# Performance work log

Measured on AMD Instinct MI355X. Metric: run time of the kernel, lower is better.

The kernel has to match this reference:

```python
import jax, jax.numpy as jnp
import numpy as np

EPS = 1e-5

def layer_norm(x, gamma, beta):
    mu = jnp.mean(x, axis=-1, keepdims=True)
    var = jnp.var(x, axis=-1, keepdims=True)
    return (x - mu) * jax.lax.rsqrt(var + EPS) * gamma + beta

def setup_inputs() -> dict:
    key = jax.random.key(0)
    ks = jax.random.split(key, 4)
    B, L, D = 32, 4096, 768
    x = jax.random.normal(ks[0], (B, L, D), dtype=jnp.float32)
    w_kv = jax.random.normal(ks[1], (2 * D, D), dtype=jnp.float32) * (D ** -0.5)
    query = jax.random.normal(ks[2], (D,), dtype=jnp.float32)
    gamma1 = jnp.ones((D,), jnp.float32)
    beta1 = jnp.zeros((D,), jnp.float32)
    gamma2 = jnp.ones((D,), jnp.float32)
    beta2 = jnp.zeros((D,), jnp.float32)
    return {"x": x, "w_kv": w_kv, "query": query,
            "gamma1": gamma1, "beta1": beta1,
            "gamma2": gamma2, "beta2": beta2}

def reference(x, w_kv, query, gamma1, beta1, gamma2, beta2):
    B, L, D = x.shape
    H = 8
    Dh = D // H
    scale = Dh ** -0.5
    xn = layer_norm(x, gamma1, beta1)                      # [B,L,D]
    kv = jnp.einsum('bld,ed->ble', xn, w_kv)               # [B,L,2D]
    k, v = jnp.split(kv, 2, axis=-1)                       # [B,L,D] each
    k = k.reshape(B, L, H, Dh)                             # [B,L,H,Dh]
    v = v.reshape(B, L, H, Dh)
    q = query.reshape(H, Dh)                               # [H,Dh]
    dots = jnp.einsum('hd,blhd->bhl', q, k) * scale        # [B,H,L]
    attn = jax.nn.softmax(dots, axis=-1)                   # [B,H,L]
    out = jnp.einsum('bhl,blhd->bhd', attn, v)             # [B,H,Dh]
    out = out.reshape(B, D)                                # [B,D]
    return layer_norm(out, gamma2, beta2)
```

## Files before the change

### kernel.cpp

```cpp
#include <hip/hip_runtime.h>
#include <stdint.h>

#define DD 768
#define HN 8
#define LL 4096
#define BB 32
#define ROWS 64
#define NBLK (BB * LL / ROWS)
#define DEPTH 6
#define PSTR 772

#define GLOBAL_AS __attribute__((address_space(1)))
#define LDS_AS    __attribute__((address_space(3)))

#define DPP_STEP(x, ctrl, rmask, bc)                                           \
  x += __int_as_float(__builtin_amdgcn_update_dpp(                             \
      0, __float_as_int(x), (ctrl), (rmask), 0xf, (bc)))

__device__ __forceinline__ void wave_sum4(float& a, float& b, float& c, float& d) {
  DPP_STEP(a, 0x111, 0xf, true);  DPP_STEP(b, 0x111, 0xf, true);
  DPP_STEP(c, 0x111, 0xf, true);  DPP_STEP(d, 0x111, 0xf, true);
  DPP_STEP(a, 0x112, 0xf, true);  DPP_STEP(b, 0x112, 0xf, true);
  DPP_STEP(c, 0x112, 0xf, true);  DPP_STEP(d, 0x112, 0xf, true);
  DPP_STEP(a, 0x114, 0xf, true);  DPP_STEP(b, 0x114, 0xf, true);
  DPP_STEP(c, 0x114, 0xf, true);  DPP_STEP(d, 0x114, 0xf, true);
  DPP_STEP(a, 0x118, 0xf, true);  DPP_STEP(b, 0x118, 0xf, true);
  DPP_STEP(c, 0x118, 0xf, true);  DPP_STEP(d, 0x118, 0xf, true);
  DPP_STEP(a, 0x142, 0xa, false); DPP_STEP(b, 0x142, 0xa, false);
  DPP_STEP(c, 0x142, 0xa, false); DPP_STEP(d, 0x142, 0xa, false);
  DPP_STEP(a, 0x143, 0xc, false); DPP_STEP(b, 0x143, 0xc, false);
  DPP_STEP(c, 0x143, 0xc, false); DPP_STEP(d, 0x143, 0xc, false);
  a = __int_as_float(__builtin_amdgcn_readlane(__float_as_int(a), 63));
  b = __int_as_float(__builtin_amdgcn_readlane(__float_as_int(b), 63));
  c = __int_as_float(__builtin_amdgcn_readlane(__float_as_int(c), 63));
  d = __int_as_float(__builtin_amdgcn_readlane(__float_as_int(d), 63));
}

__device__ __forceinline__ void wave_sum2(float& a, float& b) {
  DPP_STEP(a, 0x111, 0xf, true);  DPP_STEP(b, 0x111, 0xf, true);
  DPP_STEP(a, 0x112, 0xf, true);  DPP_STEP(b, 0x112, 0xf, true);
  DPP_STEP(a, 0x114, 0xf, true);  DPP_STEP(b, 0x114, 0xf, true);
  DPP_STEP(a, 0x118, 0xf, true);  DPP_STEP(b, 0x118, 0xf, true);
  DPP_STEP(a, 0x142, 0xa, false); DPP_STEP(b, 0x142, 0xa, false);
  DPP_STEP(a, 0x143, 0xc, false); DPP_STEP(b, 0x143, 0xc, false);
  a = __int_as_float(__builtin_amdgcn_readlane(__float_as_int(a), 63));
  b = __int_as_float(__builtin_amdgcn_readlane(__float_as_int(b), 63));
}

__global__ __launch_bounds__(256) void k_qk(const float* __restrict__ wkv,
                                            const float* __restrict__ query,
                                            const float* __restrict__ gamma1,
                                            float* __restrict__ qkraw) {
  int h = blockIdx.x / 3;
  int d = (blockIdx.x % 3) * 256 + threadIdx.x;
  const float* wbase = wkv + (size_t)h * 96 * DD + d;
  const float* qb = query + h * 96;
  float acc = 0.f;
  #pragma unroll 8
  for (int i = 0; i < 96; ++i) acc = fmaf(qb[i], wbase[(size_t)i * DD], acc);
  qkraw[h * DD + d] = acc * 0.10206207261596577f * gamma1[d];
}

__global__ __launch_bounds__(64, 2) void k_main(
    const float* __restrict__ x, const float* __restrict__ qkraw,
    float* __restrict__ part) {
  const int lane = threadIdx.x;
  __shared__ float lds[DEPTH][DD];
  float* ring = &lds[0][0];

  float4 q[HN][3];
  #pragma unroll
  for (int h = 0; h < HN; ++h)
    #pragma unroll
    for (int j = 0; j < 3; ++j)
      q[h][j] = *reinterpret_cast<const float4*>(qkraw + h * DD + j * 256 + lane * 4);
  asm volatile("s_waitcnt vmcnt(0)" ::: "memory");

  {
    float m[HN];
    #pragma unroll
    for (int h = 0; h < HN; ++h) {
      float s = 0.f;
      #pragma unroll
      for (int j = 0; j < 3; ++j)
        s += q[h][j].x + q[h][j].y + q[h][j].z + q[h][j].w;
      m[h] = s;
    }
    wave_sum4(m[0], m[1], m[2], m[3]);
    wave_sum4(m[4], m[5], m[6], m[7]);
    #pragma unroll
    for (int h = 0; h < HN; ++h) {
      float mv = m[h] * (1.f / 768.f);
      #pragma unroll
      for (int j = 0; j < 3; ++j) {
        q[h][j].x -= mv; q[h][j].y -= mv; q[h][j].z -= mv; q[h][j].w -= mv;
      }
    }
  }

  float4 S[HN][3];
  float se[HN], ch[HN];
  #pragma unroll
  for (int h = 0; h < HN; ++h) {
    se[h] = 0.f; ch[h] = 0.f;
    #pragma unroll
    for (int j = 0; j < 3; ++j) S[h][j] = make_float4(0.f, 0.f, 0.f, 0.f);
  }

  const float* gbase = x + (size_t)blockIdx.x * ROWS * DD;

  #define STAGE(R, SLOT)                                                       \
    {                                                                          \
      const float* gt = gbase + (size_t)(R) * DD;                              \
      float* db = ring + (SLOT) * DD;                                          \
      _Pragma("unroll")                                                        \
      for (int i = 0; i < 3; ++i)                                              \
        __builtin_amdgcn_global_load_lds(                                      \
            (const GLOBAL_AS uint32_t*)(gt + i * 256 + lane * 4),              \
            (LDS_AS uint32_t*)(db + i * 256), 16, 0, 0);                       \
    }

  #define COMPUTE(SLOT)                                                        \
    {                                                                          \
      const float* row = ring + (SLOT) * DD;                                   \
      float4 c0 = *reinterpret_cast<const float4*>(row + lane * 4);            \
      float4 c1 = *reinterpret_cast<const float4*>(row + 256 + lane * 4);      \
      float4 c2 = *reinterpret_cast<const float4*>(row + 512 + lane * 4);      \
      float s1 = 0.f, s2 = 0.f;                                                \
      float dt[HN];                                                            \
      _Pragma("unroll") for (int h = 0; h < HN; ++h) dt[h] = 0.f;              \
      ACC4(c0, 0) ACC4(c1, 1) ACC4(c2, 2)                                      \
      wave_sum4(s1, s2, dt[0], dt[1]);                                         \
      wave_sum4(dt[2], dt[3], dt[4], dt[5]);                                   \
      wave_sum2(dt[6], dt[7]);                                                 \
      float mu   = s1 * (1.f / 768.f);                                         \
      float var  = fmaf(-mu, mu, s2 * (1.f / 768.f));                          \
      float rstd = rsqrtf(var + 1e-5f);                                        \
      float sh   = -mu * rstd;                                                 \
      float pe   = rstd * 1.44269504f;                                         \
      _Pragma("unroll")                                                        \
      for (int h = 0; h < HN; ++h) {                                           \
        float p = exp2f(dt[h] * pe);                                           \
        se[h] += p;                                                            \
        ch[h] = fmaf(p, sh, ch[h]);                                            \
        float a = p * rstd;                                                    \
        S[h][0].x = fmaf(a, c0.x, S[h][0].x);                                  \
        S[h][0].y = fmaf(a, c0.y, S[h][0].y);                                  \
        S[h][0].z = fmaf(a, c0.z, S[h][0].z);                                  \
        S[h][0].w = fmaf(a, c0.w, S[h][0].w);                                  \
        S[h][1].x = fmaf(a, c1.x, S[h][1].x);                                  \
        S[h][1].y = fmaf(a, c1.y, S[h][1].y);                                  \
        S[h][1].z = fmaf(a, c1.z, S[h][1].z);                                  \
        S[h][1].w = fmaf(a, c1.w, S[h][1].w);                                  \
        S[h][2].x = fmaf(a, c2.x, S[h][2].x);                                  \
        S[h][2].y = fmaf(a, c2.y, S[h][2].y);                                  \
        S[h][2].z = fmaf(a, c2.z, S[h][2].z);                                  \
        S[h][2].w = fmaf(a, c2.w, S[h][2].w);                                  \
      }                                                                        \
    }

#define ACC4(cv, J)                                                            \
      s1 += cv.x + cv.y + cv.z + cv.w;                                         \
      s2 = fmaf(cv.x, cv.x, s2); s2 = fmaf(cv.y, cv.y, s2);                    \
      s2 = fmaf(cv.z, cv.z, s2); s2 = fmaf(cv.w, cv.w, s2);                    \
      _Pragma("unroll")                                                        \
      for (int h = 0; h < HN; ++h) {                                           \
        dt[h] = fmaf(cv.x, q[h][J].x, dt[h]);                                  \
        dt[h] = fmaf(cv.y, q[h][J].y, dt[h]);                                  \
        dt[h] = fmaf(cv.z, q[h][J].z, dt[h]);                                  \
        dt[h] = fmaf(cv.w, q[h][J].w, dt[h]);                                  \
      }

  STAGE(0, 0) STAGE(1, 1) STAGE(2, 2) STAGE(3, 3) STAGE(4, 4)

  int sIn = 5, sCur = 0;
  #pragma unroll 1
  for (int r = 0; r <= ROWS - 6; ++r) {
    STAGE(r + 5, sIn)
    sIn = (sIn == DEPTH - 1) ? 0 : sIn + 1;
    asm volatile("s_waitcnt vmcnt(15)" ::: "memory");
    COMPUTE(sCur)
    sCur = (sCur == DEPTH - 1) ? 0 : sCur + 1;
  }
  asm volatile("s_waitcnt vmcnt(12)" ::: "memory");
  COMPUTE(sCur) sCur = (sCur == DEPTH - 1) ? 0 : sCur + 1;
  asm volatile("s_waitcnt vmcnt(9)" ::: "memory");
  COMPUTE(sCur) sCur = (sCur == DEPTH - 1) ? 0 : sCur + 1;
  asm volatile("s_waitcnt vmcnt(6)" ::: "memory");
  COMPUTE(sCur) sCur = (sCur == DEPTH - 1) ? 0 : sCur + 1;
  asm volatile("s_waitcnt vmcnt(3)" ::: "memory");
  COMPUTE(sCur) sCur = (sCur == DEPTH - 1) ? 0 : sCur + 1;
  asm volatile("s_waitcnt vmcnt(0)" ::: "memory");
  COMPUTE(sCur)

  #undef ACC4
  #undef COMPUTE
  #undef STAGE

  float* pb = part + (size_t)blockIdx.x * (HN * PSTR);
  #pragma unroll
  for (int h = 0; h < HN; ++h) {
    #pragma unroll
    for (int j = 0; j < 3; ++j) {
      float4 v = S[h][j];
      v.x += ch[h]; v.y += ch[h]; v.z += ch[h]; v.w += ch[h];
      *reinterpret_cast<float4*>(pb + h * PSTR + j * 256 + lane * 4) = v;
    }
  }
  if (lane == 0) {
    #pragma unroll
    for (int h = 0; h < HN; ++h) pb[h * PSTR + 768] = se[h];
  }
}

__global__ __launch_bounds__(256) void k_red(const float* __restrict__ part,
                                             const float* __restrict__ gamma1,
                                             const float* __restrict__ beta1,
                                             float* __restrict__ xbar) {
  int b = blockIdx.x >> 3;
  int h = blockIdx.x & 7;
  int t = threadIdx.x;
  const int CPB = LL / ROWS;
  const float* pb = part + ((size_t)b * CPB * HN + h) * PSTR;
  float se = 0.f, a0 = 0.f, a1 = 0.f, a2 = 0.f;
  #pragma unroll 4
  for (int i = 0; i < CPB; ++i) {
    const float* P = pb + (size_t)i * HN * PSTR;
    se += P[768];
    a0 += P[t];
    a1 += P[t + 256];
    a2 += P[t + 512];
  }
  float inv = 1.f / se;
  size_t ob = ((size_t)b * HN + h) * DD;
  xbar[ob + t]       = fmaf(gamma1[t],       a0 * inv, beta1[t]);
  xbar[ob + t + 256] = fmaf(gamma1[t + 256], a1 * inv, beta1[t + 256]);
  xbar[ob + t + 512] = fmaf(gamma1[t + 512], a2 * inv, beta1[t + 512]);
}

__global__ __launch_bounds__(256) void k_proj(
    const float* __restrict__ xbar, const float* __restrict__ wkv,
    float* __restrict__ outp) {
  int b  = blockIdx.x / 3;
  int gc = blockIdx.x % 3;
  int t  = threadIdx.x;
  __shared__ float xb[HN * DD];
  #pragma unroll
  for (int k = 0; k < 24; ++k) xb[k * 256 + t] = xbar[(size_t)b * HN * DD + k * 256 + t];
  __syncthreads();

  int g = gc * 256 + t;
  int h = g / 96;
  const float4* wrow = reinterpret_cast<const float4*>(wkv + (size_t)(DD + g) * DD);
  const float* xh = xb + h * DD;
  float acc = 0.f;
  #pragma unroll 4
  for (int e = 0; e < 192; ++e) {
    float4 w = wrow[e];
    acc = fmaf(w.x, xh[e * 4 + 0], acc);
    acc = fmaf(w.y, xh[e * 4 + 1], acc);
    acc = fmaf(w.z, xh[e * 4 + 2], acc);
    acc = fmaf(w.w, xh[e * 4 + 3], acc);
  }
  outp[(size_t)b * DD + g] = acc;
}

__global__ __launch_bounds__(768) void k_ln2(
    const float* __restrict__ outp, const float* __restrict__ gamma2,
    const float* __restrict__ beta2, float* __restrict__ out) {
  int b = blockIdx.x;
  int t = threadIdx.x;
  __shared__ float rs1[12], rs2[12];
  __shared__ float smu, srstd;
  float o = outp[(size_t)b * DD + t];
  float v1 = o, v2 = o * o;
  #pragma unroll
  for (int off = 1; off < 64; off <<= 1) {
    v1 += __shfl_xor(v1, off, 64);
    v2 += __shfl_xor(v2, off, 64);
  }
  int wv = t >> 6, ln = t & 63;
  if (ln == 0) { rs1[wv] = v1; rs2[wv] = v2; }
  __syncthreads();
  if (t == 0) {
    float s1 = 0.f, s2 = 0.f;
    #pragma unroll
    for (int w = 0; w < 12; ++w) { s1 += rs1[w]; s2 += rs2[w]; }
    float mu = s1 * (1.f / 768.f);
    float var = fmaf(-mu, mu, s2 * (1.f / 768.f));
    smu = mu;
    srstd = rsqrtf(var + 1e-5f);
  }
  __syncthreads();
  out[(size_t)b * DD + t] = fmaf((o - smu) * srstd, gamma2[t], beta2[t]);
}

extern "C" void kernel_launch(void* const* d_in, const int* in_sizes, int n_in,
                              void* d_out, int out_size, void* d_ws, size_t ws_size,
                              hipStream_t stream) {
  const float* x     = (const float*)d_in[0];
  const float* wkv   = (const float*)d_in[1];
  const float* query = (const float*)d_in[2];
  const float* g1    = (const float*)d_in[3];
  const float* b1    = (const float*)d_in[4];
  const float* g2    = (const float*)d_in[5];
  const float* b2    = (const float*)d_in[6];
  float* out = (float*)d_out;
  float* ws  = (float*)d_ws;

  float* qkraw = ws;
  float* part  = ws + 8192;
  float* xbar  = part + (size_t)NBLK * HN * PSTR;
  float* outp  = xbar + (size_t)BB * HN * DD;

  k_qk  <<<24,      256, 0, stream>>>(wkv, query, g1, qkraw);
  k_main<<<NBLK,    64,  0, stream>>>(x, qkraw, part);
  k_red <<<BB * HN, 256, 0, stream>>>(part, g1, b1, xbar);
  k_proj<<<BB * 3,  256, 0, stream>>>(xbar, wkv, outp);
  k_ln2 <<<BB,      768, 0, stream>>>(outp, g2, b2, out);
}
```

Measured before the change: 188.6 us.

## Process two rows per iteration with pair-granular triple-buffered LDS staging

The main loop now handles a pair of rows per iteration. Their dot-product and moment accumulations are interleaved, and all wave reductions are batched into five full four-value DPP reductions. Staging moves from a six-slot ring of single rows to three slots of row pairs. Each slot is refilled right after it is consumed, with waitcnt thresholds adjusted to match. The aim is more instruction-level parallelism and less reduction overhead per row, at the cost of higher register pressure and a shallower effective prefetch distance.

```diff
diff --git a/kernel.cpp b/kernel.cpp
--- a/kernel.cpp
+++ b/kernel.cpp
@@ -7,7 +7,7 @@
 #define BB 32
 #define ROWS 64
 #define NBLK (BB * LL / ROWS)
-#define DEPTH 6
+#define NP (ROWS / 2)
 #define PSTR 772
 
 #define GLOBAL_AS __attribute__((address_space(1)))
@@ -36,17 +36,6 @@
   d = __int_as_float(__builtin_amdgcn_readlane(__float_as_int(d), 63));
 }
 
-__device__ __forceinline__ void wave_sum2(float& a, float& b) {
-  DPP_STEP(a, 0x111, 0xf, true);  DPP_STEP(b, 0x111, 0xf, true);
-  DPP_STEP(a, 0x112, 0xf, true);  DPP_STEP(b, 0x112, 0xf, true);
-  DPP_STEP(a, 0x114, 0xf, true);  DPP_STEP(b, 0x114, 0xf, true);
-  DPP_STEP(a, 0x118, 0xf, true);  DPP_STEP(b, 0x118, 0xf, true);
-  DPP_STEP(a, 0x142, 0xa, false); DPP_STEP(b, 0x142, 0xa, false);
-  DPP_STEP(a, 0x143, 0xc, false); DPP_STEP(b, 0x143, 0xc, false);
-  a = __int_as_float(__builtin_amdgcn_readlane(__float_as_int(a), 63));
-  b = __int_as_float(__builtin_amdgcn_readlane(__float_as_int(b), 63));
-}
-
 __global__ __launch_bounds__(256) void k_qk(const float* __restrict__ wkv,
                                             const float* __restrict__ query,
                                             const float* __restrict__ gamma1,
@@ -65,8 +54,8 @@
     const float* __restrict__ x, const float* __restrict__ qkraw,
     float* __restrict__ part) {
   const int lane = threadIdx.x;
-  __shared__ float lds[DEPTH][DD];
-  float* ring = &lds[0][0];
+  __shared__ float lds[3][2][DD];
+  float* ring = &lds[0][0][0];
 
   float4 q[HN][3];
   #pragma unroll
@@ -75,7 +64,6 @@
     for (int j = 0; j < 3; ++j)
       q[h][j] = *reinterpret_cast<const float4*>(qkraw + h * DD + j * 256 + lane * 4);
   asm volatile("s_waitcnt vmcnt(0)" ::: "memory");
-
   {
     float m[HN];
     #pragma unroll
@@ -109,93 +97,104 @@
 
   const float* gbase = x + (size_t)blockIdx.x * ROWS * DD;
 
-  #define STAGE(R, SLOT)                                                       \
+  #define STAGEP(P, SLOT)                                                      \
     {                                                                          \
-      const float* gt = gbase + (size_t)(R) * DD;                              \
-      float* db = ring + (SLOT) * DD;                                          \
+      const float* gt = gbase + (size_t)(P) * (2 * DD);                        \
+      float* db = ring + (SLOT) * (2 * DD);                                    \
       _Pragma("unroll")                                                        \
-      for (int i = 0; i < 3; ++i)                                              \
+      for (int i = 0; i < 6; ++i)                                              \
         __builtin_amdgcn_global_load_lds(                                      \
             (const GLOBAL_AS uint32_t*)(gt + i * 256 + lane * 4),              \
             (LDS_AS uint32_t*)(db + i * 256), 16, 0, 0);                       \
     }
 
-  #define COMPUTE(SLOT)                                                        \
+#define ACC4(cv, J, DT)                                                        \
+      s1 += cv.x + cv.y + cv.z + cv.w;                                         \
+      s2 = fmaf(cv.x, cv.x, s2); s2 = fmaf(cv.y, cv.y, s2);                    \
+      s2 = fmaf(cv.z, cv.z, s2); s2 = fmaf(cv.w, cv.w, s2);                    \
+      _Pragma("unroll")                                                        \
+      for (int h = 0; h < HN; ++h) {                                           \
+        DT[h] = fmaf(cv.x, q[h][J].x, DT[h]);                                  \
+        DT[h] = fmaf(cv.y, q[h][J].y, DT[h]);                                  \
+        DT[h] = fmaf(cv.z, q[h][J].z, DT[h]);                                  \
+        DT[h] = fmaf(cv.w, q[h][J].w, DT[h]);                                  \
+      }
+
+  #define TAIL(S1, S2, DT, C0, C1, C2)                                         \
     {                                                                          \
-      const float* row = ring + (SLOT) * DD;                                   \
-      float4 c0 = *reinterpret_cast<const float4*>(row + lane * 4);            \
-      float4 c1 = *reinterpret_cast<const float4*>(row + 256 + lane * 4);      \
-      float4 c2 = *reinterpret_cast<const float4*>(row + 512 + lane * 4);      \
-      float s1 = 0.f, s2 = 0.f;                                                \
-      float dt[HN];                                                            \
-      _Pragma("unroll") for (int h = 0; h < HN; ++h) dt[h] = 0.f;              \
-      ACC4(c0, 0) ACC4(c1, 1) ACC4(c2, 2)                                      \
-      wave_sum4(s1, s2, dt[0], dt[1]);                                         \
-      wave_sum4(dt[2], dt[3], dt[4], dt[5]);                                   \
-      wave_sum2(dt[6], dt[7]);                                                 \
-      float mu   = s1 * (1.f / 768.f);                                         \
-      float var  = fmaf(-mu, mu, s2 * (1.f / 768.f));                          \
+      float mu   = S1 * (1.f / 768.f);                                         \
+      float var  = fmaf(-mu, mu, S2 * (1.f / 768.f));                          \
       float rstd = rsqrtf(var + 1e-5f);                                        \
       float sh   = -mu * rstd;                                                 \
       float pe   = rstd * 1.44269504f;                                         \
       _Pragma("unroll")                                                        \
       for (int h = 0; h < HN; ++h) {                                           \
-        float p = exp2f(dt[h] * pe);                                           \
+        float p = exp2f(DT[h] * pe);                                           \
         se[h] += p;                                                            \
         ch[h] = fmaf(p, sh, ch[h]);                                            \
         float a = p * rstd;                                                    \
-        S[h][0].x = fmaf(a, c0.x, S[h][0].x);                                  \
-        S[h][0].y = fmaf(a, c0.y, S[h][0].y);                                  \
-        S[h][0].z = fmaf(a, c0.z, S[h][0].z);                                  \
-        S[h][0].w = fmaf(a, c0.w, S[h][0].w);                                  \
-        S[h][1].x = fmaf(a, c1.x, S[h][1].x);                                  \
-        S[h][1].y = fmaf(a, c1.y, S[h][1].y);                                  \
-        S[h][1].z = fmaf(a, c1.z, S[h][1].z);                                  \
-        S[h][1].w = fmaf(a, c1.w, S[h][1].w);                                  \
-        S[h][2].x = fmaf(a, c2.x, S[h][2].x);                                  \
-        S[h][2].y = fmaf(a, c2.y, S[h][2].y);                                  \
-        S[h][2].z = fmaf(a, c2.z, S[h][2].z);                                  \
-        S[h][2].w = fmaf(a, c2.w, S[h][2].w);                                  \
+        S[h][0].x = fmaf(a, C0.x, S[h][0].x);                                  \
+        S[h][0].y = fmaf(a, C0.y, S[h][0].y);                                  \
+        S[h][0].z = fmaf(a, C0.z, S[h][0].z);                                  \
+        S[h][0].w = fmaf(a, C0.w, S[h][0].w);                                  \
+        S[h][1].x = fmaf(a, C1.x, S[h][1].x);                                  \
+        S[h][1].y = fmaf(a, C1.y, S[h][1].y);                                  \
+        S[h][1].z = fmaf(a, C1.z, S[h][1].z);                                  \
+        S[h][1].w = fmaf(a, C1.w, S[h][1].w);                                  \
+        S[h][2].x = fmaf(a, C2.x, S[h][2].x);                                  \
+        S[h][2].y = fmaf(a, C2.y, S[h][2].y);                                  \
+        S[h][2].z = fmaf(a, C2.z, S[h][2].z);                                  \
+        S[h][2].w = fmaf(a, C2.w, S[h][2].w);                                  \
       }                                                                        \
     }
 
-#define ACC4(cv, J)                                                            \
-      s1 += cv.x + cv.y + cv.z + cv.w;                                         \
-      s2 = fmaf(cv.x, cv.x, s2); s2 = fmaf(cv.y, cv.y, s2);                    \
-      s2 = fmaf(cv.z, cv.z, s2); s2 = fmaf(cv.w, cv.w, s2);                    \
-      _Pragma("unroll")                                                        \
-      for (int h = 0; h < HN; ++h) {                                           \
-        dt[h] = fmaf(cv.x, q[h][J].x, dt[h]);                                  \
-        dt[h] = fmaf(cv.y, q[h][J].y, dt[h]);                                  \
-        dt[h] = fmaf(cv.z, q[h][J].z, dt[h]);                                  \
-        dt[h] = fmaf(cv.w, q[h][J].w, dt[h]);                                  \
-      }
-
-  STAGE(0, 0) STAGE(1, 1) STAGE(2, 2) STAGE(3, 3) STAGE(4, 4)
-
-  int sIn = 5, sCur = 0;
+  #define COMPUTEP(SLOT)                                                       \
+    {                                                                          \
+      const float* ra = ring + (SLOT) * (2 * DD);                              \
+      float4 a0 = *reinterpret_cast<const float4*>(ra + lane * 4);             \
+      float4 a1 = *reinterpret_cast<const float4*>(ra + 256 + lane * 4);       \
+      float4 a2 = *reinterpret_cast<const float4*>(ra + 512 + lane * 4);       \
+      float4 b0 = *reinterpret_cast<const float4*>(ra + 768 + lane * 4);       \
+      float4 b1 = *reinterpret_cast<const float4*>(ra + 1024 + lane * 4);      \
+      float4 b2 = *reinterpret_cast<const float4*>(ra + 1280 + lane * 4);      \
+      float dta[HN], dtb[HN];                                                  \
+      _Pragma("unroll") for (int h = 0; h < HN; ++h) { dta[h] = 0.f; dtb[h] = 0.f; } \
+      float s1a, s2a, s1b, s2b;                                                \
+      { float s1 = 0.f, s2 = 0.f;                                              \
+        ACC4(a0, 0, dta) ACC4(a1, 1, dta) ACC4(a2, 2, dta)                     \
+        s1a = s1; s2a = s2; }                                                  \
+      { float s1 = 0.f, s2 = 0.f;                                              \
+        ACC4(b0, 0, dtb) ACC4(b1, 1, dtb) ACC4(b2, 2, dtb)                     \
+        s1b = s1; s2b = s2; }                                                  \
+      wave_sum4(s1a, s2a, s1b, s2b);                                           \
+      wave_sum4(dta[0], dta[1], dta[2], dta[3]);                               \
+      wave_sum4(dta[4], dta[5], dta[6], dta[7]);                               \
+      wave_sum4(dtb[0], dtb[1], dtb[2], dtb[3]);                               \
+      wave_sum4(dtb[4], dtb[5], dtb[6], dtb[7]);                               \
+      TAIL(s1a, s2a, dta, a0, a1, a2)                                          \
+      TAIL(s1b, s2b, dtb, b0, b1, b2)                                          \
+    }
+
+  STAGEP(0, 0) STAGEP(1, 1) STAGEP(2, 2)
+
+  int slot = 0;
   #pragma unroll 1
-  for (int r = 0; r <= ROWS - 6; ++r) {
-    STAGE(r + 5, sIn)
-    sIn = (sIn == DEPTH - 1) ? 0 : sIn + 1;
-    asm volatile("s_waitcnt vmcnt(15)" ::: "memory");
-    COMPUTE(sCur)
-    sCur = (sCur == DEPTH - 1) ? 0 : sCur + 1;
-  }
-  asm volatile("s_waitcnt vmcnt(12)" ::: "memory");
-  COMPUTE(sCur) sCur = (sCur == DEPTH - 1) ? 0 : sCur + 1;
-  asm volatile("s_waitcnt vmcnt(9)" ::: "memory");
-  COMPUTE(sCur) sCur = (sCur == DEPTH - 1) ? 0 : sCur + 1;
+  for (int p = 0; p <= NP - 3; ++p) {
+    asm volatile("s_waitcnt vmcnt(12)" ::: "memory");
+    COMPUTEP(slot)
+    if (p + 3 < NP) STAGEP(p + 3, slot)
+    slot = (slot == 2) ? 0 : slot + 1;
+  }
   asm volatile("s_waitcnt vmcnt(6)" ::: "memory");
-  COMPUTE(sCur) sCur = (sCur == DEPTH - 1) ? 0 : sCur + 1;
-  asm volatile("s_waitcnt vmcnt(3)" ::: "memory");
-  COMPUTE(sCur) sCur = (sCur == DEPTH - 1) ? 0 : sCur + 1;
+  COMPUTEP(slot)
+  slot = (slot == 2) ? 0 : slot + 1;
   asm volatile("s_waitcnt vmcnt(0)" ::: "memory");
-  COMPUTE(sCur)
-
+  COMPUTEP(slot)
+
+  #undef COMPUTEP
+  #undef TAIL
   #undef ACC4
-  #undef COMPUTE
-  #undef STAGE
+  #undef STAGEP
 
   float* pb = part + (size_t)blockIdx.x * (HN * PSTR);
   #pragma unroll
```

After: 170.7 us. 1.11x faster.
